# Kernel tuning notes

Hardware: AMD Instinct MI355X
Metric: run time of the kernel (lower is better)

The kernel has to match this reference:

```python
import jax, jax.numpy as jnp
import numpy as np

LN_EPS = 1e-5


def _ln(h, g, b):
    mu = h.mean(-1, keepdims=True)
    var = ((h - mu) ** 2).mean(-1, keepdims=True)
    return (h - mu) / jnp.sqrt(var + LN_EPS) * g + b


def setup_inputs() -> dict:
    key = jax.random.key(0)
    ks = jax.random.split(key, 12)
    B, T, Cin, C, D, M = 16, 1024, 512, 1024, 256, 1024
    s = 0.02
    inp = {
        "x": jax.random.normal(ks[0], (B, T, Cin), jnp.float32),
        "masks": jnp.ones((B, T), jnp.float32),
        "W1": jax.random.normal(ks[1], (Cin, C), jnp.float32) * s,
        "g1": jnp.ones((C,), jnp.float32), "b1": jnp.zeros((C,), jnp.float32),
        "W2": jax.random.normal(ks[2], (C, C), jnp.float32) * s,
        "g2": jnp.ones((C,), jnp.float32), "b2": jnp.zeros((C,), jnp.float32),
        "W3": jax.random.normal(ks[3], (C, C), jnp.float32) * s,
        "g3": jnp.ones((C,), jnp.float32), "b3": jnp.zeros((C,), jnp.float32),
        "W4": jax.random.normal(ks[4], (C, C), jnp.float32) * s,
        "g4": jnp.ones((C,), jnp.float32), "b4": jnp.zeros((C,), jnp.float32),
        "W5": jax.random.normal(ks[5], (C, D), jnp.float32) * s,
        "b5": jnp.zeros((D,), jnp.float32),
        # Dirichlet(alpha=100) rows, as in the torch init: rows live on the simplex
        "embedding": jax.random.dirichlet(ks[6], jnp.full((D,), 100.0, jnp.float32), (M,)).astype(jnp.float32),
    }
    return inp


def reference(x, masks, W1, g1, b1, W2, g2, b2, W3, g3, b3, W4, g4, b4, W5, b5, embedding):
    h = jax.nn.relu(_ln(x @ W1, g1, b1))
    h = jax.nn.relu(_ln(h @ W2, g2, b2))
    h = jax.nn.relu(_ln(h @ W3, g3, b3))
    h = jax.nn.relu(_ln(h @ W4, g4, b4))
    z = h @ W5 + b5                              # [B, T, D]
    p = jax.nn.log_softmax(z, axis=-1)           # log-prob features

    B, T, D = p.shape
    p_flat = jax.lax.stop_gradient(p.reshape(-1, D))   # x.detach() in torch
    ep = jnp.exp(p_flat)                               # [N, D]
    # KL(exp(p) || e_m) summed over D, for all codes m:
    #   sum_d exp(p)*(p - log(e_m)) = rowsum(exp(p)*p) - exp(p) @ log(E)^T
    div = (ep * p_flat).sum(-1, keepdims=True) - ep @ jnp.log(embedding).T  # [N, M]
    idx = jnp.argmin(div, axis=-1)                     # [N]
    quant = jax.lax.stop_gradient(embedding[idx].reshape(B, T, D))

    # commitment loss: masked KL(exp(p) || quant.detach())
    kl = (jnp.exp(p) * (p - jnp.log(quant))).sum(-1)   # [B, T]
    loss = 0.25 * (kl * masks).mean(0).sum()

    # straight-through estimator
    q = p + jax.lax.stop_gradient(quant - p)
    return z, q, loss
```

## Files before the change

### kernel.cpp

```cpp
#include <hip/hip_runtime.h>
#include <hip/hip_bf16.h>
#include <stdint.h>

typedef __attribute__((ext_vector_type(4))) float f32x4;
typedef __attribute__((ext_vector_type(8))) __bf16 bf16x8;
typedef __attribute__((ext_vector_type(4))) __bf16 bf16x4;

#define LN_EPS 1e-5f

__device__ __forceinline__ void gload_lds16(const void* g, void* l) {
  __builtin_amdgcn_global_load_lds(
      (__attribute__((address_space(1))) void*)(uintptr_t)g,
      (__attribute__((address_space(3))) void*)(uint32_t)(uintptr_t)l,
      16, 0, 0);
}

__device__ __forceinline__ f32x4 mfma16(bf16x8 a, bf16x8 b, f32x4 c) {
  return __builtin_amdgcn_mfma_f32_16x16x32_bf16(a, b, c, 0, 0, 0);
}

__global__ __launch_bounds__(256) void k_cvt_bf16(const float* __restrict__ x,
                                                  __bf16* __restrict__ o) {
  int i = (blockIdx.x * 256 + threadIdx.x) * 8;
  f32x4 a = *(const f32x4*)(x + i);
  f32x4 b = *(const f32x4*)(x + i + 4);
  bf16x8 v;
#pragma unroll
  for (int j = 0; j < 4; ++j) { v[j] = (__bf16)a[j]; v[j + 4] = (__bf16)b[j]; }
  *(bf16x8*)(o + i) = v;
}

__global__ void k_transpose(const float* __restrict__ W, __bf16* __restrict__ Wt,
                            int K, int N) {
  __shared__ float t[32][33];
  int nt = blockIdx.x * 32, kt = blockIdx.y * 32;
  int tx = threadIdx.x, ty = threadIdx.y;
  t[ty][tx] = W[(size_t)(kt + ty) * N + nt + tx];
  __syncthreads();
  Wt[(size_t)(nt + ty) * K + kt + tx] = (__bf16)t[tx][ty];
}

__global__ void k_transpose3(const float* __restrict__ Wa, const float* __restrict__ Wb,
                             const float* __restrict__ Wc, __bf16* __restrict__ Ta,
                             __bf16* __restrict__ Tb, __bf16* __restrict__ Tc) {
  __shared__ float t[32][33];
  const float* W = blockIdx.z == 0 ? Wa : (blockIdx.z == 1 ? Wb : Wc);
  __bf16* T = blockIdx.z == 0 ? Ta : (blockIdx.z == 1 ? Tb : Tc);
  int nt = blockIdx.x * 32, kt = blockIdx.y * 32;
  int tx = threadIdx.x, ty = threadIdx.y;
  t[ty][tx] = W[(size_t)(kt + ty) * 1024 + nt + tx];
  __syncthreads();
  T[(size_t)(nt + ty) * 1024 + kt + tx] = (__bf16)t[tx][ty];
}

__global__ __launch_bounds__(256) void k_logE(const float* __restrict__ e,
                                              __bf16* __restrict__ o) {
  int i = blockIdx.x * 256 + threadIdx.x;
  o[i] = (__bf16)logf(e[i] * 256.0f);
}

__global__ __launch_bounds__(512, 2) void k_gemm256(
    const __bf16* __restrict__ A, const __bf16* __restrict__ Bt,
    __bf16* __restrict__ O, int N, int K) {
  __shared__ char lds[131072];
  const int tid = threadIdx.x;
  const int lane = tid & 63;
  const int wid = tid >> 6;
  const int wm = wid >> 2;
  const int wn = wid & 3;
  const int bm0 = blockIdx.x * 256;
  const int bn0 = blockIdx.y * 256;
  const int NT = K >> 6;

  const int slin = tid * 16;
  const int lrow = slin >> 7;
  const int scol = (slin & 127) ^ ((lrow & 7) << 4);
  const char* Ab = (const char*)A;
  const char* Bb = (const char*)Bt;
  const uint32_t rs = (uint32_t)K * 2;

  const int klo = (lane >> 4) * 16;
  const int sw = (lane & 7) << 4;
  const uint32_t kx0 = (uint32_t)(klo ^ sw);
  const uint32_t kx1 = (uint32_t)((64 + klo) ^ sw);
  const uint32_t abase = (uint32_t)(wm * 128 + (lane & 15)) * 128;
  const uint32_t bbase = (uint32_t)(wn * 64 + (lane & 15)) * 128;

  f32x4 acc[8][4];
#pragma unroll
  for (int i = 0; i < 8; ++i)
#pragma unroll
    for (int j = 0; j < 4; ++j) acc[i][j] = 0.0f;

#define LDSA(buf) (lds + (buf)*32768)
#define LDSB(buf) (lds + 65536 + (buf)*32768)
#define STAGE_A(t, h)                                                              \
  {                                                                                \
    const char* src = Ab + (size_t)(bm0 + (h)*128 + lrow) * rs + ((t) << 7) + scol;\
    char* dst = LDSA((t)&1) + (h)*16384 + slin;                                    \
    gload_lds16(src, dst);                                                         \
    gload_lds16(src + (size_t)64 * rs, dst + 8192);                                \
  }
#define STAGE_B(t, h)                                                              \
  {                                                                                \
    const char* src = Bb + (size_t)(bn0 + (h)*128 + lrow) * rs + ((t) << 7) + scol;\
    char* dst = LDSB((t)&1) + (h)*16384 + slin;                                    \
    gload_lds16(src, dst);                                                         \
    gload_lds16(src + (size_t)64 * rs, dst + 8192);                                \
  }

  STAGE_A(0, 0); STAGE_A(0, 1); STAGE_B(0, 0); STAGE_B(0, 1);
  STAGE_B(1, 0); STAGE_B(1, 1);
  asm volatile("s_waitcnt vmcnt(4)");
  __builtin_amdgcn_s_barrier();
  __builtin_amdgcn_sched_barrier(0);

  for (int t = 0; t < NT; ++t) {
    const char* Acur = LDSA(t & 1);
    const char* Bcur = LDSB(t & 1);

    if (t + 1 < NT) { STAGE_A(t + 1, 0); STAGE_A(t + 1, 1); }
    bf16x8 bF[4][2];
#pragma unroll
    for (int ni = 0; ni < 4; ++ni) {
      bF[ni][0] = *(const bf16x8*)(Bcur + bbase + ni * 2048 + kx0);
      bF[ni][1] = *(const bf16x8*)(Bcur + bbase + ni * 2048 + kx1);
    }
    {
      bf16x8 aF[4][2];
#pragma unroll
      for (int mi = 0; mi < 4; ++mi) {
        aF[mi][0] = *(const bf16x8*)(Acur + abase + mi * 2048 + kx0);
        aF[mi][1] = *(const bf16x8*)(Acur + abase + mi * 2048 + kx1);
      }
      __builtin_amdgcn_s_setprio(1);
#pragma unroll
      for (int mi = 0; mi < 4; ++mi)
#pragma unroll
        for (int ni = 0; ni < 4; ++ni) {
          acc[mi][ni] = mfma16(aF[mi][0], bF[ni][0], acc[mi][ni]);
          acc[mi][ni] = mfma16(aF[mi][1], bF[ni][1], acc[mi][ni]);
        }
      __builtin_amdgcn_s_setprio(0);
    }
    __builtin_amdgcn_s_barrier();
    __builtin_amdgcn_sched_barrier(0);

    if (t + 2 < NT) { STAGE_B(t + 2, 0); STAGE_B(t + 2, 1); }
    {
      bf16x8 aF[4][2];
#pragma unroll
      for (int mi = 0; mi < 4; ++mi) {
        aF[mi][0] = *(const bf16x8*)(Acur + abase + (mi + 4) * 2048 + kx0);
        aF[mi][1] = *(const bf16x8*)(Acur + abase + (mi + 4) * 2048 + kx1);
      }
      __builtin_amdgcn_s_setprio(1);
#pragma unroll
      for (int mi = 0; mi < 4; ++mi)
#pragma unroll
        for (int ni = 0; ni < 4; ++ni) {
          acc[mi + 4][ni] = mfma16(aF[mi][0], bF[ni][0], acc[mi + 4][ni]);
          acc[mi + 4][ni] = mfma16(aF[mi][1], bF[ni][1], acc[mi + 4][ni]);
        }
      __builtin_amdgcn_s_setprio(0);
    }
    if (t + 1 < NT) {
      asm volatile("s_waitcnt vmcnt(4)");
      __builtin_amdgcn_s_barrier();
      __builtin_amdgcn_sched_barrier(0);
    }
  }
#undef STAGE_A
#undef STAGE_B
#undef LDSA
#undef LDSB

  const int r0 = (lane >> 4) * 4;
  const int cc = lane & 15;
#pragma unroll
  for (int mi = 0; mi < 8; ++mi) {
#pragma unroll
    for (int ni = 0; ni < 4; ++ni) {
      int r = bm0 + wm * 128 + mi * 16 + r0;
      int c = bn0 + wn * 64 + ni * 16 + cc;
#pragma unroll
      for (int j = 0; j < 4; ++j)
        O[(size_t)(r + j) * N + c] = (__bf16)acc[mi][ni][j];
    }
  }
}

__global__ __launch_bounds__(256) void k_ln_relu(__bf16* __restrict__ h,
                                                 const float* __restrict__ g,
                                                 const float* __restrict__ b) {
  int lane = threadIdx.x & 63;
  int row = blockIdx.x * 4 + (threadIdx.x >> 6);
  __bf16* rp = h + (size_t)row * 1024;
  bf16x8 v0 = *(const bf16x8*)(rp + lane * 8);
  bf16x8 v1 = *(const bf16x8*)(rp + 512 + lane * 8);
  float f0[8], f1[8];
  float s = 0.f, sq = 0.f;
#pragma unroll
  for (int j = 0; j < 8; ++j) {
    f0[j] = (float)v0[j]; f1[j] = (float)v1[j];
    s += f0[j] + f1[j];
    sq += f0[j] * f0[j] + f1[j] * f1[j];
  }
#pragma unroll
  for (int d = 1; d < 64; d <<= 1) { s += __shfl_xor(s, d); sq += __shfl_xor(sq, d); }
  float mu = s * (1.0f / 1024.0f);
  float var = sq * (1.0f / 1024.0f) - mu * mu;
  float rstd = rsqrtf(var + LN_EPS);
  const f32x4* gv = (const f32x4*)g;
  const f32x4* bv = (const f32x4*)b;
  f32x4 ga0 = gv[lane * 2], ga1 = gv[lane * 2 + 1];
  f32x4 gb0 = gv[128 + lane * 2], gb1 = gv[128 + lane * 2 + 1];
  f32x4 ba0 = bv[lane * 2], ba1 = bv[lane * 2 + 1];
  f32x4 bb0 = bv[128 + lane * 2], bb1 = bv[128 + lane * 2 + 1];
  bf16x8 o0, o1;
#pragma unroll
  for (int j = 0; j < 4; ++j) {
    float t0 = (f0[j] - mu) * rstd * ga0[j] + ba0[j];
    float t1 = (f0[j + 4] - mu) * rstd * ga1[j] + ba1[j];
    float t2 = (f1[j] - mu) * rstd * gb0[j] + bb0[j];
    float t3 = (f1[j + 4] - mu) * rstd * gb1[j] + bb1[j];
    o0[j] = (__bf16)fmaxf(t0, 0.f);
    o0[j + 4] = (__bf16)fmaxf(t1, 0.f);
    o1[j] = (__bf16)fmaxf(t2, 0.f);
    o1[j + 4] = (__bf16)fmaxf(t3, 0.f);
  }
  *(bf16x8*)(rp + lane * 8) = o0;
  *(bf16x8*)(rp + 512 + lane * 8) = o1;
}

__global__ __launch_bounds__(256) void k_gemm_sm(
    const __bf16* __restrict__ A, const __bf16* __restrict__ Bt,
    const float* __restrict__ bias, float* __restrict__ z,
    __bf16* __restrict__ ep, float* __restrict__ sm) {
  const int K = 1024;
  __shared__ char lds[40960];
  char* ldsA = lds;
  char* ldsB = lds + 8192;
  const int tid = threadIdx.x;
  const int lane = tid & 63;
  const int wn = tid >> 6;
  const int bm0 = blockIdx.x * 64;
  const char* Ab = (const char*)A;
  const char* Bb = (const char*)Bt;
  const uint32_t rs = (uint32_t)K * 2;

  const int cc = lane & 15;
  uint32_t ra[2][4], rb[2][4];
  {
    const int sww = (lane & 7) << 4;
    const int gk = lane & 48;
#pragma unroll
    for (int kk = 0; kk < 2; ++kk) {
#pragma unroll
      for (int i = 0; i < 4; ++i) {
        uint32_t kb = (uint32_t)((kk * 64 + gk) ^ sww);
        ra[kk][i] = (uint32_t)(i * 16 + cc) * 128 + kb;
        rb[kk][i] = (uint32_t)(wn * 64 + i * 16 + cc) * 128 + kb;
      }
    }
  }

  f32x4 acc[4][4];
#pragma unroll
  for (int i = 0; i < 4; ++i)
#pragma unroll
    for (int j = 0; j < 4; ++j) acc[i][j] = 0.0f;

  for (int k0 = 0; k0 < K; k0 += 64) {
    __syncthreads();
#pragma unroll
    for (int i = 0; i < 2; ++i) {
      int lin = i * 4096 + tid * 16;
      int row = lin >> 7;
      int col = (lin & 127) ^ ((row & 7) << 4);
      gload_lds16(Ab + (size_t)(bm0 + row) * rs + k0 * 2 + col, ldsA + lin);
    }
#pragma unroll
    for (int i = 0; i < 8; ++i) {
      int lin = i * 4096 + tid * 16;
      int row = lin >> 7;
      int col = (lin & 127) ^ ((row & 7) << 4);
      gload_lds16(Bb + (size_t)row * rs + k0 * 2 + col, ldsB + lin);
    }
    __syncthreads();
#pragma unroll
    for (int kk = 0; kk < 2; ++kk) {
      bf16x8 af[4], bfv[4];
#pragma unroll
      for (int i = 0; i < 4; ++i) af[i] = *(const bf16x8*)(ldsA + ra[kk][i]);
#pragma unroll
      for (int i = 0; i < 4; ++i) bfv[i] = *(const bf16x8*)(ldsB + rb[kk][i]);
#pragma unroll
      for (int mi = 0; mi < 4; ++mi)
#pragma unroll
        for (int ni = 0; ni < 4; ++ni)
          acc[mi][ni] = mfma16(af[mi], bfv[ni], acc[mi][ni]);
    }
  }

  __syncthreads();
  float* stm = (float*)lds;
  float* sts = (float*)(lds + 1024);
  float* rowm = (float*)(lds + 2048);
  float* rows_ = (float*)(lds + 2304);

  const int r0 = (lane >> 4) * 4;
  float bvv[4];
#pragma unroll
  for (int ni = 0; ni < 4; ++ni) bvv[ni] = bias[wn * 64 + ni * 16 + cc];

#pragma unroll
  for (int mi = 0; mi < 4; ++mi) {
#pragma unroll
    for (int j = 0; j < 4; ++j) {
      float m = -3.4e38f;
#pragma unroll
      for (int ni = 0; ni < 4; ++ni) m = fmaxf(m, acc[mi][ni][j] + bvv[ni]);
#pragma unroll
      for (int d = 1; d < 16; d <<= 1) m = fmaxf(m, __shfl_xor(m, d));
      if (cc == 0) stm[wn * 64 + mi * 16 + r0 + j] = m;
    }
  }
  __syncthreads();
  if (tid < 64) {
    float m = fmaxf(fmaxf(stm[tid], stm[64 + tid]), fmaxf(stm[128 + tid], stm[192 + tid]));
    rowm[tid] = m;
  }
  __syncthreads();
#pragma unroll
  for (int mi = 0; mi < 4; ++mi) {
#pragma unroll
    for (int j = 0; j < 4; ++j) {
      int r = mi * 16 + r0 + j;
      float m = rowm[r];
      float s = 0.f;
#pragma unroll
      for (int ni = 0; ni < 4; ++ni) s += expf(acc[mi][ni][j] + bvv[ni] - m);
#pragma unroll
      for (int d = 1; d < 16; d <<= 1) s += __shfl_xor(s, d);
      if (cc == 0) sts[wn * 64 + r] = s;
    }
  }
  __syncthreads();
  if (tid < 64) {
    float s = sts[tid] + sts[64 + tid] + sts[128 + tid] + sts[192 + tid];
    rows_[tid] = s;
    sm[bm0 + tid] = rowm[tid] + logf(s);
  }
  __syncthreads();
#pragma unroll
  for (int mi = 0; mi < 4; ++mi) {
#pragma unroll
    for (int j = 0; j < 4; ++j) {
      int r = mi * 16 + r0 + j;
      float m = rowm[r];
      float inv = 1.0f / rows_[r];
      float* zp = z + (size_t)(bm0 + r) * 256;
      __bf16* epp = ep + (size_t)(bm0 + r) * 256;
#pragma unroll
      for (int ni = 0; ni < 4; ++ni) {
        int c = wn * 64 + ni * 16 + cc;
        float zz = acc[mi][ni][j] + bvv[ni];
        zp[c] = zz;
        epp[c] = (__bf16)(expf(zz - m) * inv);
      }
    }
  }
}

__global__ __launch_bounds__(256) void k_gemm_div(
    const __bf16* __restrict__ A, const __bf16* __restrict__ Bt,
    float* __restrict__ part_val, int* __restrict__ part_idx, int N, int K) {
  __shared__ char lds[32768];
  char* ldsA = lds;
  char* ldsB = lds + 16384;
  const int tid = threadIdx.x;
  const int lane = tid & 63;
  const int wid = tid >> 6;
  const int wm = wid >> 1, wn = wid & 1;
  const int bm0 = blockIdx.x * 128;
  const int bn0 = blockIdx.y * 128;

  const int slin = tid * 16;
  const int srow = slin >> 7;
  const int scol = (slin & 127) ^ ((srow & 7) << 4);

  const char* Ab = (const char*)A;
  const char* Bb = (const char*)Bt;
  const uint32_t rs = (uint32_t)K * 2;

  uint32_t ra[2][4], rb[2][4];
  {
    const int sw = (lane & 7) << 4;
    const int gk = lane & 48;
#pragma unroll
    for (int kk = 0; kk < 2; ++kk) {
#pragma unroll
      for (int i = 0; i < 4; ++i) {
        uint32_t kb = (uint32_t)((kk * 64 + gk) ^ sw);
        ra[kk][i] = (uint32_t)(wm * 64 + i * 16 + (lane & 15)) * 128 + kb;
        rb[kk][i] = (uint32_t)(wn * 64 + i * 16 + (lane & 15)) * 128 + kb;
      }
    }
  }

  f32x4 acc[4][4];
#pragma unroll
  for (int i = 0; i < 4; ++i)
#pragma unroll
    for (int j = 0; j < 4; ++j) acc[i][j] = 0.0f;

  for (int k0 = 0; k0 < K; k0 += 64) {
    __syncthreads();
    const uint32_t kbyte = (uint32_t)k0 * 2 + (uint32_t)scol;
#pragma unroll
    for (int i = 0; i < 4; ++i) {
      int row = i * 32 + srow;
      gload_lds16(Ab + (size_t)(bm0 + row) * rs + kbyte, ldsA + i * 4096 + slin);
    }
#pragma unroll
    for (int i = 0; i < 4; ++i) {
      int row = i * 32 + srow;
      gload_lds16(Bb + (size_t)(bn0 + row) * rs + kbyte, ldsB + i * 4096 + slin);
    }
    __syncthreads();
#pragma unroll
    for (int kk = 0; kk < 2; ++kk) {
      bf16x8 af[4], bfv[4];
#pragma unroll
      for (int i = 0; i < 4; ++i) af[i] = *(const bf16x8*)(ldsA + ra[kk][i]);
#pragma unroll
      for (int i = 0; i < 4; ++i) bfv[i] = *(const bf16x8*)(ldsB + rb[kk][i]);
#pragma unroll
      for (int mi = 0; mi < 4; ++mi)
#pragma unroll
        for (int ni = 0; ni < 4; ++ni)
          acc[mi][ni] = mfma16(af[mi], bfv[ni], acc[mi][ni]);
    }
  }

  const int r0 = (lane >> 4) * 4;
  const int cc = lane & 15;
  const int nch = N >> 6;
#pragma unroll
  for (int mi = 0; mi < 4; ++mi) {
#pragma unroll
    for (int j = 0; j < 4; ++j) {
      float v = acc[mi][0][j];
      int c = cc;
#pragma unroll
      for (int ni = 1; ni < 4; ++ni) {
        float v2 = acc[mi][ni][j];
        int c2 = ni * 16 + cc;
        if (v2 > v) { v = v2; c = c2; }
      }
#pragma unroll
      for (int d = 1; d < 16; d <<= 1) {
        float ov = __shfl_xor(v, d);
        int oc = __shfl_xor(c, d);
        if (ov > v || (ov == v && oc < c)) { v = ov; c = oc; }
      }
      if (cc == 0) {
        int r = bm0 + wm * 64 + mi * 16 + r0 + j;
        int chunk = (bn0 >> 6) + wn;
        part_val[r * nch + chunk] = v;
        part_idx[r * nch + chunk] = bn0 + wn * 64 + c;
      }
    }
  }
}

__global__ __launch_bounds__(256) void k_final(
    const float* __restrict__ part_val, const int* __restrict__ part_idx,
    const float* __restrict__ z, const float* __restrict__ sm,
    const float* __restrict__ emb, const float* __restrict__ masks,
    float* __restrict__ q, float* __restrict__ blockloss) {
  __shared__ float ls[4];
  int lane = threadIdx.x & 63;
  int w = threadIdx.x >> 6;
  int row = blockIdx.x * 4 + w;
  float v = -3.4e38f;
  int c = 0x7fffffff;
  if (lane < 16) { v = part_val[row * 16 + lane]; c = part_idx[row * 16 + lane]; }
#pragma unroll
  for (int d = 1; d < 16; d <<= 1) {
    float ov = __shfl_xor(v, d);
    int oc = __shfl_xor(c, d);
    if (ov > v || (ov == v && oc < c)) { v = ov; c = oc; }
  }
  int code = __shfl(c, 0);
  f32x4 ev = ((const f32x4*)(emb + (size_t)code * 256))[lane];
  ((f32x4*)(q + (size_t)row * 256))[lane] = ev;
  f32x4 zv = ((const f32x4*)(z + (size_t)row * 256))[lane];
  float smr = sm[row];
  float kl = 0.f;
#pragma unroll
  for (int j = 0; j < 4; ++j) {
    float pj = zv[j] - smr;
    kl += expf(pj) * (pj - logf(ev[j]));
  }
#pragma unroll
  for (int d = 1; d < 64; d <<= 1) kl += __shfl_xor(kl, d);
  if (lane == 0) ls[w] = kl * masks[row];
  __syncthreads();
  if (threadIdx.x == 0) blockloss[blockIdx.x] = ls[0] + ls[1] + ls[2] + ls[3];
}

__global__ __launch_bounds__(256) void k_loss_reduce(const float* __restrict__ bl,
                                                     float* __restrict__ out) {
  __shared__ float s[256];
  float a = 0.f;
#pragma unroll
  for (int i = 0; i < 16; ++i) a += bl[threadIdx.x + i * 256];
  s[threadIdx.x] = a;
  __syncthreads();
  for (int st = 128; st > 0; st >>= 1) {
    if (threadIdx.x < st) s[threadIdx.x] += s[threadIdx.x + st];
    __syncthreads();
  }
  if (threadIdx.x == 0) out[0] = s[0] * (0.25f / 16.0f);
}

extern "C" void kernel_launch(void* const* d_in, const int* in_sizes, int n_in,
                              void* d_out, int out_size, void* d_ws, size_t ws_size,
                              hipStream_t stream) {
  const float* x = (const float*)d_in[0];
  const float* masks = (const float*)d_in[1];
  const float* W1 = (const float*)d_in[2];
  const float* g1 = (const float*)d_in[3];
  const float* b1 = (const float*)d_in[4];
  const float* W2 = (const float*)d_in[5];
  const float* g2 = (const float*)d_in[6];
  const float* b2 = (const float*)d_in[7];
  const float* W3 = (const float*)d_in[8];
  const float* g3 = (const float*)d_in[9];
  const float* b3 = (const float*)d_in[10];
  const float* W4 = (const float*)d_in[11];
  const float* g4 = (const float*)d_in[12];
  const float* b4 = (const float*)d_in[13];
  const float* W5 = (const float*)d_in[14];
  const float* b5 = (const float*)d_in[15];
  const float* emb = (const float*)d_in[16];

  const int M = 16384;
  char* ws = (char*)d_ws;
  __bf16* bufA = (__bf16*)(ws);
  __bf16* bufB = (__bf16*)(ws + (32ull << 20));
  __bf16* W1t = (__bf16*)(ws + (64ull << 20));
  __bf16* W2t = (__bf16*)(ws + (65ull << 20));
  __bf16* W3t = (__bf16*)(ws + (67ull << 20));
  __bf16* W4t = (__bf16*)(ws + (69ull << 20));
  __bf16* W5t = (__bf16*)(ws + (71ull << 20));
  __bf16* logE = (__bf16*)(ws + (72ull << 20));
  float* part_val = (float*)(ws + (73ull << 20));
  int* part_idx = (int*)(ws + (74ull << 20));
  float* blockloss = (float*)(ws + (75ull << 20));
  float* sm = (float*)(ws + (76ull << 20));
  __bf16* ep = (__bf16*)(ws + (16ull << 20));

  float* z = (float*)d_out;
  float* q = z + (size_t)M * 256;
  float* lossp = z + 2ull * M * 256;

  dim3 tb32(32, 32);
  k_cvt_bf16<<<4096, 256, 0, stream>>>(x, bufB);
  k_transpose<<<dim3(32, 16), tb32, 0, stream>>>(W1, W1t, 512, 1024);
  k_transpose3<<<dim3(32, 32, 3), tb32, 0, stream>>>(W2, W3, W4, W2t, W3t, W4t);
  k_transpose<<<dim3(8, 32), tb32, 0, stream>>>(W5, W5t, 1024, 256);
  k_logE<<<1024, 256, 0, stream>>>(emb, logE);

  k_gemm256<<<dim3(64, 4), 512, 0, stream>>>(bufB, W1t, bufA, 1024, 512);
  k_ln_relu<<<4096, 256, 0, stream>>>(bufA, g1, b1);
  k_gemm256<<<dim3(64, 4), 512, 0, stream>>>(bufA, W2t, bufB, 1024, 1024);
  k_ln_relu<<<4096, 256, 0, stream>>>(bufB, g2, b2);
  k_gemm256<<<dim3(64, 4), 512, 0, stream>>>(bufB, W3t, bufA, 1024, 1024);
  k_ln_relu<<<4096, 256, 0, stream>>>(bufA, g3, b3);
  k_gemm256<<<dim3(64, 4), 512, 0, stream>>>(bufA, W4t, bufB, 1024, 1024);
  k_ln_relu<<<4096, 256, 0, stream>>>(bufB, g4, b4);
  k_gemm_sm<<<256, 256, 0, stream>>>(bufB, W5t, b5, z, ep, sm);
  k_gemm_div<<<dim3(128, 8), 256, 0, stream>>>(ep, logE, part_val, part_idx, 1024, 256);
  k_final<<<4096, 256, 0, stream>>>(part_val, part_idx, z, sm, emb, masks, q, blockloss);
  k_loss_reduce<<<1, 256, 0, stream>>>(blockloss, lossp);
}
```

Measured before the change: 271.0 us.

## Fuse last LayerNorm into GEMM epilogue/prologue and reuse big GEMM for divergence

The fourth GEMM now emits per-row partial sum and sum-of-squares from its epilogue. The W5 GEMM applies LayerNorm+ReLU to its A tile while staging it into LDS, which removes one standalone ln_relu pass over the 16384x1024 activation. The separate divergence GEMM is replaced by the 256x256-tile GEMM template with an argmax epilogue, and the pipelining waits get extra sched barriers plus a vmcnt(0) on the last tile. This trades computing variance as E[x²]-mu² (bf16 output, less numerically robust) and register-path A loads for one fewer memory pass and kernel launch.

```diff
diff --git a/kernel.cpp b/kernel.cpp
--- a/kernel.cpp
+++ b/kernel.cpp
@@ -3,6 +3,7 @@
 #include <stdint.h>
 
 typedef __attribute__((ext_vector_type(4))) float f32x4;
+typedef __attribute__((ext_vector_type(2))) float f32x2;
 typedef __attribute__((ext_vector_type(8))) __bf16 bf16x8;
 typedef __attribute__((ext_vector_type(4))) __bf16 bf16x4;
 
@@ -59,9 +60,11 @@
   o[i] = (__bf16)logf(e[i] * 256.0f);
 }
 
+template <int EPI>
 __global__ __launch_bounds__(512, 2) void k_gemm256(
     const __bf16* __restrict__ A, const __bf16* __restrict__ Bt,
-    __bf16* __restrict__ O, int N, int K) {
+    __bf16* __restrict__ O, f32x2* __restrict__ outPart,
+    float* __restrict__ part_val, int* __restrict__ part_idx, int N, int K) {
   __shared__ char lds[131072];
   const int tid = threadIdx.x;
   const int lane = tid & 63;
@@ -120,6 +123,7 @@
     const char* Bcur = LDSB(t & 1);
 
     if (t + 1 < NT) { STAGE_A(t + 1, 0); STAGE_A(t + 1, 1); }
+    __builtin_amdgcn_sched_barrier(0);
     bf16x8 bF[4][2];
 #pragma unroll
     for (int ni = 0; ni < 4; ++ni) {
@@ -147,6 +151,7 @@
     __builtin_amdgcn_sched_barrier(0);
 
     if (t + 2 < NT) { STAGE_B(t + 2, 0); STAGE_B(t + 2, 1); }
+    __builtin_amdgcn_sched_barrier(0);
     {
       bf16x8 aF[4][2];
 #pragma unroll
@@ -165,7 +170,8 @@
       __builtin_amdgcn_s_setprio(0);
     }
     if (t + 1 < NT) {
-      asm volatile("s_waitcnt vmcnt(4)");
+      if (t + 2 < NT) { asm volatile("s_waitcnt vmcnt(4)"); }
+      else            { asm volatile("s_waitcnt vmcnt(0)"); }
       __builtin_amdgcn_s_barrier();
       __builtin_amdgcn_sched_barrier(0);
     }
@@ -177,6 +183,70 @@
 
   const int r0 = (lane >> 4) * 4;
   const int cc = lane & 15;
+
+  if constexpr (EPI == 2) {
+    const int nch = N >> 6;
+    const int chunk = (bn0 >> 6) + wn;
+#pragma unroll
+    for (int mi = 0; mi < 8; ++mi) {
+#pragma unroll
+      for (int j = 0; j < 4; ++j) {
+        float v = acc[mi][0][j];
+        int c = cc;
+#pragma unroll
+        for (int ni = 1; ni < 4; ++ni) {
+          float v2 = acc[mi][ni][j];
+          int c2 = ni * 16 + cc;
+          if (v2 > v) { v = v2; c = c2; }
+        }
+#pragma unroll
+        for (int d = 1; d < 16; d <<= 1) {
+          float ov = __shfl_xor(v, d);
+          int oc = __shfl_xor(c, d);
+          if (ov > v || (ov == v && oc < c)) { v = ov; c = oc; }
+        }
+        if (cc == 0) {
+          int r = bm0 + wm * 128 + mi * 16 + r0 + j;
+          part_val[r * nch + chunk] = v;
+          part_idx[r * nch + chunk] = bn0 + wn * 64 + c;
+        }
+      }
+    }
+    return;
+  }
+
+  if constexpr (EPI == 1) {
+    __builtin_amdgcn_s_barrier();
+    float* stp = (float*)lds;
+    float* stq = (float*)(lds + 4096);
+#pragma unroll
+    for (int mi = 0; mi < 8; ++mi) {
+#pragma unroll
+      for (int j = 0; j < 4; ++j) {
+        float s = 0.f, q = 0.f;
+#pragma unroll
+        for (int ni = 0; ni < 4; ++ni) {
+          float v = acc[mi][ni][j];
+          s += v; q += v * v;
+        }
+#pragma unroll
+        for (int d = 1; d < 16; d <<= 1) { s += __shfl_xor(s, d); q += __shfl_xor(q, d); }
+        if (cc == 0) {
+          int rl = wm * 128 + mi * 16 + r0 + j;
+          stp[rl * 4 + wn] = s;
+          stq[rl * 4 + wn] = q;
+        }
+      }
+    }
+    __syncthreads();
+    if (tid < 256) {
+      float s = stp[tid * 4] + stp[tid * 4 + 1] + stp[tid * 4 + 2] + stp[tid * 4 + 3];
+      float q = stq[tid * 4] + stq[tid * 4 + 1] + stq[tid * 4 + 2] + stq[tid * 4 + 3];
+      f32x2 pr; pr[0] = s; pr[1] = q;
+      outPart[(size_t)(bm0 + tid) * 4 + blockIdx.y] = pr;
+    }
+  }
+
 #pragma unroll
   for (int mi = 0; mi < 8; ++mi) {
 #pragma unroll
@@ -235,10 +305,12 @@
 
 __global__ __launch_bounds__(256) void k_gemm_sm(
     const __bf16* __restrict__ A, const __bf16* __restrict__ Bt,
-    const float* __restrict__ bias, float* __restrict__ z,
-    __bf16* __restrict__ ep, float* __restrict__ sm) {
+    const float* __restrict__ gw, const float* __restrict__ bw,
+    const f32x2* __restrict__ inPart, const float* __restrict__ bias,
+    float* __restrict__ z, __bf16* __restrict__ ep, float* __restrict__ sm) {
   const int K = 1024;
-  __shared__ char lds[40960];
+  __shared__ char lds[49152];
+  const int GBS = 40960;
   char* ldsA = lds;
   char* ldsB = lds + 8192;
   const int tid = threadIdx.x;
@@ -248,8 +320,28 @@
   const char* Ab = (const char*)A;
   const char* Bb = (const char*)Bt;
   const uint32_t rs = (uint32_t)K * 2;
-
   const int cc = lane & 15;
+
+  ((f32x4*)(lds + GBS))[tid] = ((const f32x4*)gw)[tid];
+  ((f32x4*)(lds + GBS + 4096))[tid] = ((const f32x4*)bw)[tid];
+
+  const int ar0 = tid >> 3;
+  float aS[2], cS[2];
+#pragma unroll
+  for (int i = 0; i < 2; ++i) {
+    int r = bm0 + ar0 + i * 32;
+    const f32x4* pp = (const f32x4*)(inPart + (size_t)r * 4);
+    f32x4 p0 = pp[0], p1 = pp[1];
+    float s = p0[0] + p0[2] + p1[0] + p1[2];
+    float q = p0[1] + p0[3] + p1[1] + p1[3];
+    float mu = s * (1.0f / 1024.0f);
+    float var = q * (1.0f / 1024.0f) - mu * mu;
+    float rstd = rsqrtf(var + LN_EPS);
+    aS[i] = rstd; cS[i] = -mu * rstd;
+  }
+  const uint32_t acolb = (uint32_t)(tid & 7) * 16;
+  const uint32_t awcol = acolb ^ (uint32_t)((ar0 & 7) << 4);
+
   uint32_t ra[2][4], rb[2][4];
   {
     const int sww = (lane & 7) << 4;
@@ -273,19 +365,35 @@
 
   for (int k0 = 0; k0 < K; k0 += 64) {
     __syncthreads();
-#pragma unroll
-    for (int i = 0; i < 2; ++i) {
-      int lin = i * 4096 + tid * 16;
-      int row = lin >> 7;
-      int col = (lin & 127) ^ ((row & 7) << 4);
-      gload_lds16(Ab + (size_t)(bm0 + row) * rs + k0 * 2 + col, ldsA + lin);
-    }
+    const char* abase_ = Ab + (size_t)(bm0 + ar0) * rs + (size_t)k0 * 2 + acolb;
+    bf16x8 a0 = *(const bf16x8*)abase_;
+    bf16x8 a1 = *(const bf16x8*)(abase_ + (size_t)32 * rs);
+    __builtin_amdgcn_sched_barrier(0);
 #pragma unroll
     for (int i = 0; i < 8; ++i) {
       int lin = i * 4096 + tid * 16;
       int row = lin >> 7;
       int col = (lin & 127) ^ ((row & 7) << 4);
       gload_lds16(Bb + (size_t)row * rs + k0 * 2 + col, ldsB + lin);
+    }
+    __builtin_amdgcn_sched_barrier(0);
+    asm volatile("s_waitcnt vmcnt(8)");
+    {
+      uint32_t gb_ = GBS + (uint32_t)k0 * 4 + (uint32_t)(tid & 7) * 32;
+      f32x4 g0 = *(const f32x4*)(lds + gb_), g1 = *(const f32x4*)(lds + gb_ + 16);
+      f32x4 b0 = *(const f32x4*)(lds + gb_ + 4096), b1 = *(const f32x4*)(lds + gb_ + 4112);
+      bf16x8 o0, o1;
+#pragma unroll
+      for (int e = 0; e < 8; ++e) {
+        float ge = e < 4 ? g0[e] : g1[e - 4];
+        float be = e < 4 ? b0[e] : b1[e - 4];
+        float t0 = fmaf(fmaf((float)a0[e], aS[0], cS[0]), ge, be);
+        float t1 = fmaf(fmaf((float)a1[e], aS[1], cS[1]), ge, be);
+        o0[e] = (__bf16)fmaxf(t0, 0.f);
+        o1[e] = (__bf16)fmaxf(t1, 0.f);
+      }
+      *(bf16x8*)(ldsA + ar0 * 128 + awcol) = o0;
+      *(bf16x8*)(ldsA + (ar0 + 32) * 128 + awcol) = o1;
     }
     __syncthreads();
 #pragma unroll
@@ -368,108 +476,6 @@
         float zz = acc[mi][ni][j] + bvv[ni];
         zp[c] = zz;
         epp[c] = (__bf16)(expf(zz - m) * inv);
-      }
-    }
-  }
-}
-
-__global__ __launch_bounds__(256) void k_gemm_div(
-    const __bf16* __restrict__ A, const __bf16* __restrict__ Bt,
-    float* __restrict__ part_val, int* __restrict__ part_idx, int N, int K) {
-  __shared__ char lds[32768];
-  char* ldsA = lds;
-  char* ldsB = lds + 16384;
-  const int tid = threadIdx.x;
-  const int lane = tid & 63;
-  const int wid = tid >> 6;
-  const int wm = wid >> 1, wn = wid & 1;
-  const int bm0 = blockIdx.x * 128;
-  const int bn0 = blockIdx.y * 128;
-
-  const int slin = tid * 16;
-  const int srow = slin >> 7;
-  const int scol = (slin & 127) ^ ((srow & 7) << 4);
-
-  const char* Ab = (const char*)A;
-  const char* Bb = (const char*)Bt;
-  const uint32_t rs = (uint32_t)K * 2;
-
-  uint32_t ra[2][4], rb[2][4];
-  {
-    const int sw = (lane & 7) << 4;
-    const int gk = lane & 48;
-#pragma unroll
-    for (int kk = 0; kk < 2; ++kk) {
-#pragma unroll
-      for (int i = 0; i < 4; ++i) {
-        uint32_t kb = (uint32_t)((kk * 64 + gk) ^ sw);
-        ra[kk][i] = (uint32_t)(wm * 64 + i * 16 + (lane & 15)) * 128 + kb;
-        rb[kk][i] = (uint32_t)(wn * 64 + i * 16 + (lane & 15)) * 128 + kb;
-      }
-    }
-  }
-
-  f32x4 acc[4][4];
-#pragma unroll
-  for (int i = 0; i < 4; ++i)
-#pragma unroll
-    for (int j = 0; j < 4; ++j) acc[i][j] = 0.0f;
-
-  for (int k0 = 0; k0 < K; k0 += 64) {
-    __syncthreads();
-    const uint32_t kbyte = (uint32_t)k0 * 2 + (uint32_t)scol;
-#pragma unroll
-    for (int i = 0; i < 4; ++i) {
-      int row = i * 32 + srow;
-      gload_lds16(Ab + (size_t)(bm0 + row) * rs + kbyte, ldsA + i * 4096 + slin);
-    }
-#pragma unroll
-    for (int i = 0; i < 4; ++i) {
-      int row = i * 32 + srow;
-      gload_lds16(Bb + (size_t)(bn0 + row) * rs + kbyte, ldsB + i * 4096 + slin);
-    }
-    __syncthreads();
-#pragma unroll
-    for (int kk = 0; kk < 2; ++kk) {
-      bf16x8 af[4], bfv[4];
-#pragma unroll
-      for (int i = 0; i < 4; ++i) af[i] = *(const bf16x8*)(ldsA + ra[kk][i]);
-#pragma unroll
-      for (int i = 0; i < 4; ++i) bfv[i] = *(const bf16x8*)(ldsB + rb[kk][i]);
-#pragma unroll
-      for (int mi = 0; mi < 4; ++mi)
-#pragma unroll
-        for (int ni = 0; ni < 4; ++ni)
-          acc[mi][ni] = mfma16(af[mi], bfv[ni], acc[mi][ni]);
-    }
-  }
-
-  const int r0 = (lane >> 4) * 4;
-  const int cc = lane & 15;
-  const int nch = N >> 6;
-#pragma unroll
-  for (int mi = 0; mi < 4; ++mi) {
-#pragma unroll
-    for (int j = 0; j < 4; ++j) {
-      float v = acc[mi][0][j];
-      int c = cc;
-#pragma unroll
-      for (int ni = 1; ni < 4; ++ni) {
-        float v2 = acc[mi][ni][j];
-        int c2 = ni * 16 + cc;
-        if (v2 > v) { v = v2; c = c2; }
-      }
-#pragma unroll
-      for (int d = 1; d < 16; d <<= 1) {
-        float ov = __shfl_xor(v, d);
-        int oc = __shfl_xor(c, d);
-        if (ov > v || (ov == v && oc < c)) { v = ov; c = oc; }
-      }
-      if (cc == 0) {
-        int r = bm0 + wm * 64 + mi * 16 + r0 + j;
-        int chunk = (bn0 >> 6) + wn;
-        part_val[r * nch + chunk] = v;
-        part_idx[r * nch + chunk] = bn0 + wn * 64 + c;
       }
     }
   }
@@ -561,6 +567,7 @@
   int* part_idx = (int*)(ws + (74ull << 20));
   float* blockloss = (float*)(ws + (75ull << 20));
   float* sm = (float*)(ws + (76ull << 20));
+  f32x2* partB = (f32x2*)(ws + (78ull << 20));
   __bf16* ep = (__bf16*)(ws + (16ull << 20));
 
   float* z = (float*)d_out;
@@ -574,16 +581,15 @@
   k_transpose<<<dim3(8, 32), tb32, 0, stream>>>(W5, W5t, 1024, 256);
   k_logE<<<1024, 256, 0, stream>>>(emb, logE);
 
-  k_gemm256<<<dim3(64, 4), 512, 0, stream>>>(bufB, W1t, bufA, 1024, 512);
+  k_gemm256<0><<<dim3(64, 4), 512, 0, stream>>>(bufB, W1t, bufA, nullptr, nullptr, nullptr, 1024, 512);
   k_ln_relu<<<4096, 256, 0, stream>>>(bufA, g1, b1);
-  k_gemm256<<<dim3(64, 4), 512, 0, stream>>>(bufA, W2t, bufB, 1024, 1024);
+  k_gemm256<0><<<dim3(64, 4), 512, 0, stream>>>(bufA, W2t, bufB, nullptr, nullptr, nullptr, 1024, 1024);
   k_ln_relu<<<4096, 256, 0, stream>>>(bufB, g2, b2);
-  k_gemm256<<<dim3(64, 4), 512, 0, stream>>>(bufB, W3t, bufA, 1024, 1024);
+  k_gemm256<0><<<dim3(64, 4), 512, 0, stream>>>(bufB, W3t, bufA, nullptr, nullptr, nullptr, 1024, 1024);
   k_ln_relu<<<4096, 256, 0, stream>>>(bufA, g3, b3);
-  k_gemm256<<<dim3(64, 4), 512, 0, stream>>>(bufA, W4t, bufB, 1024, 1024);
-  k_ln_relu<<<4096, 256, 0, stream>>>(bufB, g4, b4);
-  k_gemm_sm<<<256, 256, 0, stream>>>(bufB, W5t, b5, z, ep, sm);
-  k_gemm_div<<<dim3(128, 8), 256, 0, stream>>>(ep, logE, part_val, part_idx, 1024, 256);
+  k_gemm256<1><<<dim3(64, 4), 512, 0, stream>>>(bufA, W4t, bufB, partB, nullptr, nullptr, 1024, 1024);
+  k_gemm_sm<<<256, 256, 0, stream>>>(bufB, W5t, g4, b4, partB, b5, z, ep, sm);
+  k_gemm256<2><<<dim3(64, 4), 512, 0, stream>>>(ep, logE, nullptr, nullptr, part_val, part_idx, 1024, 256);
   k_final<<<4096, 256, 0, stream>>>(part_val, part_idx, z, sm, emb, masks, q, blockloss);
   k_loss_reduce<<<1, 256, 0, stream>>>(blockloss, lossp);
 }
```

Result: faster. 262.0 us (-3.3%).
